# Performance work log

Measured on AMD Instinct MI355X. Metric: run time of the kernel, lower is better.

## Reference

```python
import jax, jax.numpy as jnp
import numpy as np

N_EMBED = 1024
N_HEAD = 16
B, T = 4, 2048
EPS = 1e-5


def setup_inputs() -> dict:
    key = jax.random.key(0)
    ks = jax.random.split(key, 8)
    s = 0.02
    return {
        "x": jax.random.normal(ks[0], (B, T, N_EMBED), dtype=jnp.float32),
        "ln1_w": jnp.ones((N_EMBED,), jnp.float32),
        "ln1_b": jnp.zeros((N_EMBED,), jnp.float32),
        "w_qkv": jax.random.normal(ks[1], (N_EMBED, 3 * N_EMBED), dtype=jnp.float32) * s,
        "b_qkv": jnp.zeros((3 * N_EMBED,), jnp.float32),
        "w_o": jax.random.normal(ks[2], (N_EMBED, N_EMBED), dtype=jnp.float32) * s,
        "b_o": jnp.zeros((N_EMBED,), jnp.float32),
        "ln2_w": jnp.ones((N_EMBED,), jnp.float32),
        "ln2_b": jnp.zeros((N_EMBED,), jnp.float32),
        "w_fc": jax.random.normal(ks[3], (N_EMBED, 4 * N_EMBED), dtype=jnp.float32) * s,
        "b_fc": jnp.zeros((4 * N_EMBED,), jnp.float32),
        "w_proj": jax.random.normal(ks[4], (4 * N_EMBED, N_EMBED), dtype=jnp.float32) * s,
        "b_proj": jnp.zeros((N_EMBED,), jnp.float32),
    }


def _layernorm(x, w, b):
    mu = jnp.mean(x, axis=-1, keepdims=True)
    var = jnp.mean(jnp.square(x - mu), axis=-1, keepdims=True)
    return (x - mu) * jax.lax.rsqrt(var + EPS) * w + b


def _attention(x, w_qkv, b_qkv, w_o, b_o):
    b, t, c = x.shape
    hd = c // N_HEAD
    qkv = x @ w_qkv + b_qkv                      # [B,T,3C]
    q, k, v = jnp.split(qkv, 3, axis=-1)
    # [B,H,T,hd]
    q = q.reshape(b, t, N_HEAD, hd).transpose(0, 2, 1, 3)
    k = k.reshape(b, t, N_HEAD, hd).transpose(0, 2, 1, 3)
    v = v.reshape(b, t, N_HEAD, hd).transpose(0, 2, 1, 3)
    scale = 1.0 / np.sqrt(hd).astype(np.float32)
    scores = jnp.einsum('bhqd,bhkd->bhqk', q, k) * scale  # [B,H,T,T]
    mask = jnp.tril(jnp.ones((t, t), dtype=bool))
    scores = jnp.where(mask, scores, -jnp.inf)
    attn = jax.nn.softmax(scores, axis=-1)
    ctx = jnp.einsum('bhqk,bhkd->bhqd', attn, v)  # [B,H,T,hd]
    ctx = ctx.transpose(0, 2, 1, 3).reshape(b, t, c)
    return ctx @ w_o + b_o


def reference(x, ln1_w, ln1_b, w_qkv, b_qkv, w_o, b_o,
              ln2_w, ln2_b, w_fc, b_fc, w_proj, b_proj):
    # x = x + attn(ln1(x))
    x = x + _attention(_layernorm(x, ln1_w, ln1_b), w_qkv, b_qkv, w_o, b_o)
    # x = x + mlp(ln2(x))
    h = _layernorm(x, ln2_w, ln2_b)
    h = jax.nn.gelu(h @ w_fc + b_fc, approximate=False)
    x = x + (h @ w_proj + b_proj)
    return x
```

## Files before the change

kernel.cpp:

```cpp
#include <hip/hip_runtime.h>
#include <hip/hip_bf16.h>
#include <math.h>

#define N_EMBED 1024
#define N_HEAD 16
#define HD 64
#define BB 4
#define TT 2048
#define NTOK (BB * TT)
#define QKV_LD (3 * N_EMBED)

typedef __bf16 bf16x8 __attribute__((ext_vector_type(8)));
typedef float f32x4 __attribute__((ext_vector_type(4)));

__device__ __forceinline__ unsigned short f2bf(float f) {
    __hip_bfloat16 h = __float2bfloat16(f);
    return __builtin_bit_cast(unsigned short, h);
}

__device__ __forceinline__ void gll16(const unsigned short* g, unsigned short* l) {
    __builtin_amdgcn_global_load_lds(
        (const __attribute__((address_space(1))) void*)g,
        (__attribute__((address_space(3))) void*)l,
        16, 0, 0);
}

__global__ __launch_bounds__(256) void transpose_bf16_kernel(
    const float* __restrict__ in, unsigned short* __restrict__ out, int K, int N) {
    __shared__ float tile[32][33];
    int bx = blockIdx.x * 32;
    int by = blockIdx.y * 32;
    int tx = threadIdx.x, ty = threadIdx.y;
#pragma unroll
    for (int i = ty; i < 32; i += 8)
        tile[i][tx] = in[(size_t)(by + i) * N + bx + tx];
    __syncthreads();
#pragma unroll
    for (int i = ty; i < 32; i += 8)
        out[(size_t)(bx + i) * K + by + tx] = f2bf(tile[tx][i]);
}

__global__ __launch_bounds__(256) void transpose_v_kernel(
    const unsigned short* __restrict__ qkv, unsigned short* __restrict__ vt) {
    __shared__ unsigned short tile[32][33];
    int z = blockIdx.z;
    int b = z >> 4, h = z & 15;
    int t0 = blockIdx.x * 32, d0 = blockIdx.y * 32;
    int tx = threadIdx.x, ty = threadIdx.y;
    const unsigned short* src = qkv + (size_t)(b * TT) * QKV_LD + 2 * N_EMBED + h * HD;
#pragma unroll
    for (int i = ty; i < 32; i += 8)
        tile[i][tx] = src[(size_t)(t0 + i) * QKV_LD + d0 + tx];
    __syncthreads();
    unsigned short* dst = vt + (size_t)z * HD * TT;
#pragma unroll
    for (int i = ty; i < 32; i += 8)
        dst[(size_t)(d0 + i) * TT + t0 + tx] = tile[tx][i];
}

__global__ __launch_bounds__(256) void ln_kernel(
    const float* __restrict__ x, const float* __restrict__ w,
    const float* __restrict__ b, unsigned short* __restrict__ out) {
    int row = blockIdx.x;
    int t = threadIdx.x;
    const float* xr = x + (size_t)row * N_EMBED;
    float4 v = reinterpret_cast<const float4*>(xr)[t];
    float s = v.x + v.y + v.z + v.w;
    float s2 = v.x * v.x + v.y * v.y + v.z * v.z + v.w * v.w;
#pragma unroll
    for (int m = 1; m < 64; m <<= 1) {
        s += __shfl_xor(s, m);
        s2 += __shfl_xor(s2, m);
    }
    __shared__ float red[8];
    int wv = t >> 6, ln = t & 63;
    if (ln == 0) { red[wv] = s; red[wv + 4] = s2; }
    __syncthreads();
    s = red[0] + red[1] + red[2] + red[3];
    s2 = red[4] + red[5] + red[6] + red[7];
    float mu = s * (1.0f / N_EMBED);
    float var = s2 * (1.0f / N_EMBED) - mu * mu;
    float r = rsqrtf(var + 1e-5f);
    float4 wv4 = reinterpret_cast<const float4*>(w)[t];
    float4 bv4 = reinterpret_cast<const float4*>(b)[t];
    ushort4 o;
    o.x = f2bf((v.x - mu) * r * wv4.x + bv4.x);
    o.y = f2bf((v.y - mu) * r * wv4.y + bv4.y);
    o.z = f2bf((v.z - mu) * r * wv4.z + bv4.z);
    o.w = f2bf((v.w - mu) * r * wv4.w + bv4.w);
    *reinterpret_cast<ushort4*>(out + (size_t)row * N_EMBED + t * 4) = o;
}

template <int EPI>
__global__ __launch_bounds__(256) void gemm_kernel(
    const unsigned short* __restrict__ A,
    const unsigned short* __restrict__ BT,
    const float* __restrict__ bias,
    const float* __restrict__ resid,
    float* __restrict__ outf,
    unsigned short* __restrict__ outb,
    int M, int N, int K) {
    __shared__ __align__(16) unsigned short As[2][128 * 32];
    __shared__ __align__(16) unsigned short Bs[2][128 * 32];
    int nbn = N >> 7;
    int nwg = gridDim.x;
    int orig = blockIdx.x;
    int swz = (orig & 7) * (nwg >> 3) + (orig >> 3);
    int bm = swz / nbn, bn = swz % nbn;
    int t = threadIdx.x;
    int lane = t & 63, wv = t >> 6;
    int wm = wv >> 1, wn = wv & 1;
    int mr = lane & 15, kg = lane >> 4;

    f32x4 acc[4][4];
#pragma unroll
    for (int i = 0; i < 4; i++)
#pragma unroll
        for (int j = 0; j < 4; j++) acc[i][j] = (f32x4){0.f, 0.f, 0.f, 0.f};

    int srow = t >> 2, sq = t & 3;
    const unsigned short* gA1 = A + (size_t)(bm * 128 + srow) * K + sq * 8;
    const unsigned short* gA2 = gA1 + (size_t)64 * K;
    const unsigned short* gB1 = BT + (size_t)(bn * 128 + srow) * K + sq * 8;
    const unsigned short* gB2 = gB1 + (size_t)64 * K;
    int w512 = wv * 512;

    gll16(gA1, As[0] + w512);
    gll16(gA2, As[0] + 2048 + w512);
    gll16(gB1, Bs[0] + w512);
    gll16(gB2, Bs[0] + 2048 + w512);
    __syncthreads();

    int nk = K >> 5;
    for (int ki = 0; ki < nk; ki++) {
        int cur = ki & 1;
        if (ki + 1 < nk) {
            int k0 = (ki + 1) << 5;
            gll16(gA1 + k0, As[cur ^ 1] + w512);
            gll16(gA2 + k0, As[cur ^ 1] + 2048 + w512);
            gll16(gB1 + k0, Bs[cur ^ 1] + w512);
            gll16(gB2 + k0, Bs[cur ^ 1] + 2048 + w512);
        }
        bf16x8 af[4], bfr[4];
#pragma unroll
        for (int i = 0; i < 4; i++)
            af[i] = *reinterpret_cast<const bf16x8*>(&As[cur][(wm * 64 + i * 16 + mr) * 32 + kg * 8]);
#pragma unroll
        for (int j = 0; j < 4; j++)
            bfr[j] = *reinterpret_cast<const bf16x8*>(&Bs[cur][(wn * 64 + j * 16 + mr) * 32 + kg * 8]);
#pragma unroll
        for (int i = 0; i < 4; i++)
#pragma unroll
            for (int j = 0; j < 4; j++)
                acc[i][j] = __builtin_amdgcn_mfma_f32_16x16x32_bf16(af[i], bfr[j], acc[i][j], 0, 0, 0);
        __syncthreads();
    }

#pragma unroll
    for (int i = 0; i < 4; i++)
#pragma unroll
        for (int j = 0; j < 4; j++) {
            int n = bn * 128 + wn * 64 + j * 16 + mr;
            float bs = bias[n];
#pragma unroll
            for (int r = 0; r < 4; r++) {
                int m = bm * 128 + wm * 64 + i * 16 + kg * 4 + r;
                size_t idx = (size_t)m * N + n;
                float v = acc[i][j][r] + bs;
                if (EPI == 0) {
                    outb[idx] = f2bf(v);
                } else if (EPI == 1) {
                    outf[idx] = v + resid[idx];
                } else {
                    float g = 0.5f * v * (1.0f + erff(v * 0.70710678118f));
                    outb[idx] = f2bf(g);
                }
            }
        }
}

__global__ __launch_bounds__(256) void attn_kernel(
    const unsigned short* __restrict__ qkv,
    const unsigned short* __restrict__ vt,
    unsigned short* __restrict__ ctx) {
    __shared__ __align__(16) unsigned short Kb[3][4096];
    __shared__ __align__(16) unsigned short Vb[3][4096];
    __shared__ __align__(16) unsigned short PT[8192];
    const float SCL = 0.18033688011112042f;
    int t = threadIdx.x, lane = t & 63, wv = t >> 6;
    int mr = lane & 15, kg = lane >> 4;

    int wid = blockIdx.x;
    int bh = wid & 63, qp2 = wid >> 6;
    int h = bh & 15, b = bh >> 4;

    const unsigned short* qptr = qkv + (size_t)(b * TT) * QKV_LD + h * HD;
    const unsigned short* kp = qptr + N_EMBED;
    const unsigned short* vtp = vt + (size_t)bh * HD * TT;

    int srow[2], scol[2], sbase[2];
#pragma unroll
    for (int i = 0; i < 2; i++) {
        int L = i * 256 + wv * 64 + lane;
        int row = L >> 3, slot = L & 7;
        srow[i] = row;
        scol[i] = (slot ^ (row & 7)) * 8;
        sbase[i] = (i * 256 + wv * 64) * 8;
    }
    const int csw = mr & 7;

    auto stage = [&](int tile, int bi) {
        int kv0 = tile * 64;
#pragma unroll
        for (int i = 0; i < 2; i++) {
            gll16(kp + (size_t)(kv0 + srow[i]) * QKV_LD + scol[i], &Kb[bi][sbase[i]]);
            gll16(vtp + (size_t)srow[i] * TT + kv0 + scol[i], &Vb[bi][sbase[i]]);
        }
    };

    for (int item = 0; item < 2; ++item) {
        int qt = (item == 0) ? qp2 : 15 - qp2;
        int ntiles = 2 * qt + 2;
        int qbase = qt * 128 + wv * 32;

        bf16x8 aq[2][2];
#pragma unroll
        for (int f = 0; f < 2; f++)
#pragma unroll
            for (int c = 0; c < 2; c++)
                aq[f][c] = *reinterpret_cast<const bf16x8*>(
                    qptr + (size_t)(qbase + f * 16 + mr) * QKV_LD + c * 32 + kg * 8);

        f32x4 Oa[2][4];
#pragma unroll
        for (int f = 0; f < 2; f++)
#pragma unroll
            for (int jd = 0; jd < 4; jd++) Oa[f][jd] = (f32x4){0.f, 0.f, 0.f, 0.f};
        float mrow[2] = {-3.0e38f, -3.0e38f};
        float lrow[2] = {0.f, 0.f};

        stage(0, 0);
        stage(1, 1);

        for (int tl = 0; tl < ntiles; ++tl) {
            if (tl + 1 < ntiles) {
                asm volatile("s_waitcnt vmcnt(4)" ::: "memory");
            } else {
                asm volatile("s_waitcnt vmcnt(0)" ::: "memory");
            }
            __builtin_amdgcn_s_barrier();
            int t2 = tl + 2;
            if (t2 < ntiles) stage(t2, t2 % 3);

            int bi = tl % 3;
            int kv0 = tl * 64;
            const unsigned short* Kt = Kb[bi];
            const unsigned short* Vt = Vb[bi];

            f32x4 sf[2][4];
#pragma unroll
            for (int j = 0; j < 4; j++) {
                int rl = j * 16 + mr;
                bf16x8 bk0 = *reinterpret_cast<const bf16x8*>(&Kt[rl * 64 + (kg ^ csw) * 8]);
                bf16x8 bk1 = *reinterpret_cast<const bf16x8*>(&Kt[rl * 64 + ((4 + kg) ^ csw) * 8]);
#pragma unroll
                for (int f = 0; f < 2; f++) {
                    f32x4 s = (f32x4){0.f, 0.f, 0.f, 0.f};
                    s = __builtin_amdgcn_mfma_f32_16x16x32_bf16(bk0, aq[f][0], s, 0, 0, 0);
                    s = __builtin_amdgcn_mfma_f32_16x16x32_bf16(bk1, aq[f][1], s, 0, 0, 0);
                    sf[f][j] = s;
                }
            }

            bool dmask = (tl >= 2 * qt);
#pragma unroll
            for (int f = 0; f < 2; f++) {
                int qrow = qbase + f * 16 + mr;
                int R = wv * 32 + f * 16 + mr;
                float mx = -3.0e38f;
#pragma unroll
                for (int j = 0; j < 4; j++)
#pragma unroll
                    for (int r = 0; r < 4; r++) {
                        float sv = sf[f][j][r] * SCL;
                        if (dmask && (kv0 + j * 16 + kg * 4 + r > qrow)) sv = -3.0e38f;
                        sf[f][j][r] = sv;
                        mx = fmaxf(mx, sv);
                    }
                mx = fmaxf(mx, __shfl_xor(mx, 16));
                mx = fmaxf(mx, __shfl_xor(mx, 32));
                float mn = fmaxf(mrow[f], mx);
                float al = __builtin_amdgcn_exp2f(mrow[f] - mn);
                mrow[f] = mn;
#pragma unroll
                for (int jd = 0; jd < 4; jd++) Oa[f][jd] *= al;
                float ps = 0.f;
#pragma unroll
                for (int j = 0; j < 4; j++)
#pragma unroll
                    for (int r = 0; r < 4; r++) {
                        float p = __builtin_amdgcn_exp2f(sf[f][j][r] - mn);
                        sf[f][j][r] = p;
                        ps += p;
                    }
                ps += __shfl_xor(ps, 16);
                ps += __shfl_xor(ps, 32);
                lrow[f] = lrow[f] * al + ps;
                int rsw = R & 7;
#pragma unroll
                for (int j = 0; j < 4; j++) {
                    unsigned lo = (unsigned)f2bf(sf[f][j][0]) | ((unsigned)f2bf(sf[f][j][1]) << 16);
                    unsigned hi = (unsigned)f2bf(sf[f][j][2]) | ((unsigned)f2bf(sf[f][j][3]) << 16);
                    int cw = 2 * j + (kg >> 1);
                    int addr = R * 64 + ((cw ^ rsw) << 3) + (kg & 1) * 4;
                    uint2 pk; pk.x = lo; pk.y = hi;
                    *reinterpret_cast<uint2*>(&PT[addr]) = pk;
                }
            }

#pragma unroll
            for (int c = 0; c < 2; c++) {
                int R0 = wv * 32 + mr, R1 = R0 + 16;
                bf16x8 pb0 = *reinterpret_cast<const bf16x8*>(
                    &PT[R0 * 64 + (((c * 4 + kg) ^ (R0 & 7)) << 3)]);
                bf16x8 pb1 = *reinterpret_cast<const bf16x8*>(
                    &PT[R1 * 64 + (((c * 4 + kg) ^ (R1 & 7)) << 3)]);
#pragma unroll
                for (int jd = 0; jd < 4; jd++) {
                    int rv = jd * 16 + mr;
                    bf16x8 vf = *reinterpret_cast<const bf16x8*>(
                        &Vt[rv * 64 + (((c * 4 + kg) ^ (rv & 7)) << 3)]);
                    Oa[0][jd] = __builtin_amdgcn_mfma_f32_16x16x32_bf16(vf, pb0, Oa[0][jd], 0, 0, 0);
                    Oa[1][jd] = __builtin_amdgcn_mfma_f32_16x16x32_bf16(vf, pb1, Oa[1][jd], 0, 0, 0);
                }
            }
        }

#pragma unroll
        for (int f = 0; f < 2; f++) {
            float iv = 1.0f / lrow[f];
            int q = qbase + f * 16 + mr;
#pragma unroll
            for (int jd = 0; jd < 4; jd++) {
                ushort4 o;
                o.x = f2bf(Oa[f][jd][0] * iv);
                o.y = f2bf(Oa[f][jd][1] * iv);
                o.z = f2bf(Oa[f][jd][2] * iv);
                o.w = f2bf(Oa[f][jd][3] * iv);
                *reinterpret_cast<ushort4*>(
                    ctx + (size_t)(b * TT + q) * N_EMBED + h * HD + jd * 16 + kg * 4) = o;
            }
        }
        __syncthreads();
    }
}

extern "C" void kernel_launch(void* const* d_in, const int* in_sizes, int n_in,
                              void* d_out, int out_size, void* d_ws, size_t ws_size,
                              hipStream_t stream) {
    const float* x      = (const float*)d_in[0];
    const float* ln1_w  = (const float*)d_in[1];
    const float* ln1_b  = (const float*)d_in[2];
    const float* w_qkv  = (const float*)d_in[3];
    const float* b_qkv  = (const float*)d_in[4];
    const float* w_o    = (const float*)d_in[5];
    const float* b_o    = (const float*)d_in[6];
    const float* ln2_w  = (const float*)d_in[7];
    const float* ln2_b  = (const float*)d_in[8];
    const float* w_fc   = (const float*)d_in[9];
    const float* b_fc   = (const float*)d_in[10];
    const float* w_proj = (const float*)d_in[11];
    const float* b_proj = (const float*)d_in[12];
    float* out = (float*)d_out;

    char* ws = (char*)d_ws;
    size_t off = 0;
    auto alloc = [&](size_t bytes) -> void* {
        void* p = ws + off;
        off += (bytes + 255) & ~(size_t)255;
        return p;
    };
    unsigned short* wqkv_t  = (unsigned short*)alloc((size_t)3072 * 1024 * 2);
    unsigned short* wo_t    = (unsigned short*)alloc((size_t)1024 * 1024 * 2);
    unsigned short* wfc_t   = (unsigned short*)alloc((size_t)4096 * 1024 * 2);
    unsigned short* wproj_t = (unsigned short*)alloc((size_t)1024 * 4096 * 2);
    unsigned short* lnb     = (unsigned short*)alloc((size_t)NTOK * 1024 * 2);
    float*          x1      = (float*)alloc((size_t)NTOK * 1024 * 4);
    unsigned short* qkv     = (unsigned short*)alloc((size_t)NTOK * 3072 * 2);
    unsigned short* ctxb    = (unsigned short*)alloc((size_t)NTOK * 1024 * 2);
    unsigned short* hbuf    = qkv;
    unsigned short* vt      = (unsigned short*)x1;

    dim3 tb32(32, 8);
    transpose_bf16_kernel<<<dim3(3072 / 32, 1024 / 32), tb32, 0, stream>>>(w_qkv, wqkv_t, 1024, 3072);
    transpose_bf16_kernel<<<dim3(1024 / 32, 1024 / 32), tb32, 0, stream>>>(w_o, wo_t, 1024, 1024);
    transpose_bf16_kernel<<<dim3(4096 / 32, 1024 / 32), tb32, 0, stream>>>(w_fc, wfc_t, 1024, 4096);
    transpose_bf16_kernel<<<dim3(1024 / 32, 4096 / 32), tb32, 0, stream>>>(w_proj, wproj_t, 4096, 1024);

    ln_kernel<<<NTOK, 256, 0, stream>>>(x, ln1_w, ln1_b, lnb);
    gemm_kernel<0><<<(NTOK / 128) * (3072 / 128), 256, 0, stream>>>(
        lnb, wqkv_t, b_qkv, nullptr, nullptr, qkv, NTOK, 3072, 1024);
    transpose_v_kernel<<<dim3(TT / 32, HD / 32, BB * N_HEAD), tb32, 0, stream>>>(qkv, vt);
    attn_kernel<<<512, 256, 0, stream>>>(qkv, vt, ctxb);
    gemm_kernel<1><<<(NTOK / 128) * (1024 / 128), 256, 0, stream>>>(
        ctxb, wo_t, b_o, x, x1, nullptr, NTOK, 1024, 1024);
    ln_kernel<<<NTOK, 256, 0, stream>>>(x1, ln2_w, ln2_b, lnb);
    gemm_kernel<2><<<(NTOK / 128) * (4096 / 128), 256, 0, stream>>>(
        lnb, wfc_t, b_fc, nullptr, nullptr, hbuf, NTOK, 4096, 1024);
    gemm_kernel<1><<<(NTOK / 128) * (1024 / 128), 256, 0, stream>>>(
        hbuf, wproj_t, b_proj, x1, out, nullptr, NTOK, 1024, 4096);
}
```

Baseline: 426.0 us.

## Triple-buffer GEMM LDS tiles with vmcnt waits and XOR-swizzled layout

Moves the GEMM main loop from double to triple buffering in LDS, issuing global-to-LDS loads two K-steps ahead. A single barrier per iteration is gated by explicit s_waitcnt vmcnt counts, so load latency overlaps with MFMA work. An XOR swizzle on the 16-byte column chunk is applied to both the global source addresses and the LDS fragment reads to cut LDS bank conflicts. This uses more LDS per block, which may limit occupancy, and depends on the vmcnt accounting being correct.

```diff
diff --git a/kernel.cpp b/kernel.cpp
--- a/kernel.cpp
+++ b/kernel.cpp
@@ -100,8 +100,8 @@
     float* __restrict__ outf,
     unsigned short* __restrict__ outb,
     int M, int N, int K) {
-    __shared__ __align__(16) unsigned short As[2][128 * 32];
-    __shared__ __align__(16) unsigned short Bs[2][128 * 32];
+    __shared__ __align__(16) unsigned short As[3][128 * 32];
+    __shared__ __align__(16) unsigned short Bs[3][128 * 32];
     int nbn = N >> 7;
     int nwg = gridDim.x;
     int orig = blockIdx.x;
@@ -119,41 +119,50 @@
         for (int j = 0; j < 4; j++) acc[i][j] = (f32x4){0.f, 0.f, 0.f, 0.f};
 
     int srow = t >> 2, sq = t & 3;
-    const unsigned short* gA1 = A + (size_t)(bm * 128 + srow) * K + sq * 8;
+    int sqs = sq ^ ((srow >> 1) & 3);
+    const unsigned short* gA1 = A + (size_t)(bm * 128 + srow) * K + sqs * 8;
     const unsigned short* gA2 = gA1 + (size_t)64 * K;
-    const unsigned short* gB1 = BT + (size_t)(bn * 128 + srow) * K + sq * 8;
+    const unsigned short* gB1 = BT + (size_t)(bn * 128 + srow) * K + sqs * 8;
     const unsigned short* gB2 = gB1 + (size_t)64 * K;
     int w512 = wv * 512;
 
-    gll16(gA1, As[0] + w512);
-    gll16(gA2, As[0] + 2048 + w512);
-    gll16(gB1, Bs[0] + w512);
-    gll16(gB2, Bs[0] + 2048 + w512);
-    __syncthreads();
+    auto stageg = [&](int ki, int bi) {
+        int k0 = ki << 5;
+        gll16(gA1 + k0, As[bi] + w512);
+        gll16(gA2 + k0, As[bi] + 2048 + w512);
+        gll16(gB1 + k0, Bs[bi] + w512);
+        gll16(gB2 + k0, Bs[bi] + 2048 + w512);
+    };
 
     int nk = K >> 5;
+    stageg(0, 0);
+    stageg(1, 1);
+
+    const int csw = (mr >> 1) & 3;
     for (int ki = 0; ki < nk; ki++) {
-        int cur = ki & 1;
         if (ki + 1 < nk) {
-            int k0 = (ki + 1) << 5;
-            gll16(gA1 + k0, As[cur ^ 1] + w512);
-            gll16(gA2 + k0, As[cur ^ 1] + 2048 + w512);
-            gll16(gB1 + k0, Bs[cur ^ 1] + w512);
-            gll16(gB2 + k0, Bs[cur ^ 1] + 2048 + w512);
+            asm volatile("s_waitcnt vmcnt(4)" ::: "memory");
+        } else {
+            asm volatile("s_waitcnt vmcnt(0)" ::: "memory");
         }
+        __builtin_amdgcn_s_barrier();
+        if (ki + 2 < nk) stageg(ki + 2, (ki + 2) % 3);
+
+        int cur = ki % 3;
         bf16x8 af[4], bfr[4];
 #pragma unroll
         for (int i = 0; i < 4; i++)
-            af[i] = *reinterpret_cast<const bf16x8*>(&As[cur][(wm * 64 + i * 16 + mr) * 32 + kg * 8]);
+            af[i] = *reinterpret_cast<const bf16x8*>(
+                &As[cur][(wm * 64 + i * 16 + mr) * 32 + ((kg ^ csw) * 8)]);
 #pragma unroll
         for (int j = 0; j < 4; j++)
-            bfr[j] = *reinterpret_cast<const bf16x8*>(&Bs[cur][(wn * 64 + j * 16 + mr) * 32 + kg * 8]);
+            bfr[j] = *reinterpret_cast<const bf16x8*>(
+                &Bs[cur][(wn * 64 + j * 16 + mr) * 32 + ((kg ^ csw) * 8)]);
 #pragma unroll
         for (int i = 0; i < 4; i++)
 #pragma unroll
             for (int j = 0; j < 4; j++)
                 acc[i][j] = __builtin_amdgcn_mfma_f32_16x16x32_bf16(af[i], bfr[j], acc[i][j], 0, 0, 0);
-        __syncthreads();
     }
 
 #pragma unroll
```

Measured after the change: 425.1 us (median of 3 runs). Within noise of the previous version (-0.2%).
